# Optimization experiments

Hardware: AMD Instinct MI355X
Metric: run time of the kernel (lower is better)

The kernel has to match this reference:

```python
import jax, jax.numpy as jnp
import numpy as np

H = 16          # head_count
D = 1024        # model_dim
DPH = D // H    # dim_per_head


def setup_inputs() -> dict:
    key0 = jax.random.key(0)
    ks = jax.random.split(key0, 13)
    B, S = 4, 2048
    scale = 1.0 / np.sqrt(D)
    inp = {
        "key": jax.random.normal(ks[0], (B, S, D), jnp.float32),
        "value": jax.random.normal(ks[1], (B, S, D), jnp.float32),
        "query": jax.random.normal(ks[2], (B, S, D), jnp.float32),
        "mask": jax.random.randint(ks[3], (B, S, S), 0, 2).astype(jnp.bool_),
        "Wq": jax.random.normal(ks[4], (D, D), jnp.float32) * scale,
        "bq": jnp.zeros((D,), jnp.float32),
        "Wk": jax.random.normal(ks[5], (D, D), jnp.float32) * scale,
        "bk": jnp.zeros((D,), jnp.float32),
        "Wv": jax.random.normal(ks[6], (D, D), jnp.float32) * scale,
        "bv": jnp.zeros((D,), jnp.float32),
        "Wo": jax.random.normal(ks[7], (D, D), jnp.float32) * scale,
        "bo": jnp.zeros((D,), jnp.float32),
    }
    return inp


def _shape(x, B):
    # [B, S, D] -> [B, H, S, DPH]
    return x.reshape(B, -1, H, DPH).transpose(0, 2, 1, 3)


def reference(key, value, query, mask, Wq, bq, Wk, bk, Wv, bv, Wo, bo):
    B, S, _ = key.shape
    k_up = _shape(key @ Wk + bk, B)                       # [B,H,S,DPH]
    v_up = _shape(value @ Wv + bv, B)                     # [B,H,S,DPH]
    q_up = _shape(query @ Wq + bq, B) / jnp.sqrt(jnp.asarray(DPH, key.dtype))
    scores = jnp.einsum('bhqd,bhkd->bhqk', q_up, k_up)    # [B,H,S,S]
    scores = jnp.where(mask[:, None, :, :], jnp.asarray(-1e18, scores.dtype), scores)
    attn = jax.nn.softmax(scores, axis=-1)                # dropout = identity (eval)
    context = jnp.einsum('bhqk,bhkd->bhqd', attn, v_up)   # [B,H,S,DPH]
    context = context.transpose(0, 2, 1, 3).reshape(B, S, H * DPH)
    return context @ Wo + bo
```

## Files before the change

kernel.cpp:

```cpp
#include <hip/hip_runtime.h>

typedef _Float16 half8 __attribute__((ext_vector_type(8)));
typedef _Float16 half4 __attribute__((ext_vector_type(4)));
typedef float floatx4 __attribute__((ext_vector_type(4)));
typedef float floatx16 __attribute__((ext_vector_type(16)));

#define MFMA16(A,B,C) __builtin_amdgcn_mfma_f32_16x16x32_f16((A),(B),(C),0,0,0)
#define MFMA32(A,B,C) __builtin_amdgcn_mfma_f32_32x32x16_f16((A),(B),(C),0,0,0)


__global__ __launch_bounds__(256) void maskpack(
    const int* __restrict__ m, unsigned int* __restrict__ p)
{
  const int w = blockIdx.x * 256 + threadIdx.x;
  const int b = w >> 17;
  const int rem = w & 131071;
  const int s = rem >> 6;
  const int wp = rem & 63;
  const int4* src = (const int4*)(m + (size_t)w * 32);
  unsigned int bits = 0;
#pragma unroll
  for (int j = 0; j < 8; ++j) {
    const int4 v = src[j];
    bits |= (v.x ? 1u : 0u) << (j * 4 + 0);
    bits |= (v.y ? 1u : 0u) << (j * 4 + 1);
    bits |= (v.z ? 1u : 0u) << (j * 4 + 2);
    bits |= (v.w ? 1u : 0u) << (j * 4 + 3);
  }
  p[((size_t)(b * 64 + wp)) * 2048 + s] = bits;
}

__global__ __launch_bounds__(256) void wconv(
    const float* __restrict__ Wq, const float* __restrict__ Wk,
    const float* __restrict__ Wv, const float* __restrict__ Wo,
    _Float16* __restrict__ dst)
{
  const float* W = (blockIdx.z == 0) ? Wq : (blockIdx.z == 1) ? Wk
                  : (blockIdx.z == 2) ? Wv : Wo;
  _Float16* WT = dst + (size_t)blockIdx.z * 1024 * 1024;
  __shared__ float t[32][33];
  const int tx = threadIdx.x & 31;
  const int ty = threadIdx.x >> 5;
  const int k0 = blockIdx.x * 32, n0 = blockIdx.y * 32;
#pragma unroll
  for (int j = 0; j < 4; ++j)
    t[ty + j * 8][tx] = W[(size_t)(k0 + ty + j * 8) * 1024 + n0 + tx];
  __syncthreads();
#pragma unroll
  for (int j = 0; j < 4; ++j)
    WT[(size_t)(n0 + ty + j * 8) * 1024 + k0 + tx] = (_Float16)t[tx][ty + j * 8];
}

template <int OP>
__global__ __launch_bounds__(256) void gemm_k(
    const void* __restrict__ Ap, const _Float16* __restrict__ BT,
    const float* __restrict__ bias, void* __restrict__ Cp)
{
  __shared__ __align__(16) _Float16 As[128 * 64];
  __shared__ __align__(16) _Float16 Bs[128 * 64];
  const int tid = threadIdx.x;
  const int lane = tid & 63;
  const int wv = tid >> 6;
  const int m0 = blockIdx.x * 128;
  const int n0 = blockIdx.y * 128;
  const int wr = (wv >> 1) * 64;
  const int wc = (wv & 1) * 64;

  floatx4 acc[4][4];
#pragma unroll
  for (int i = 0; i < 4; ++i)
#pragma unroll
    for (int j = 0; j < 4; ++j) acc[i][j] = (floatx4){0.f, 0.f, 0.f, 0.f};

  char* AsB = (char*)As;
  char* BsB = (char*)Bs;

  for (int ko = 0; ko < 1024; ko += 64) {
#pragma unroll
    for (int r = 0; r < 4; ++r) {
      const int idx = (r * 256 + tid) * 8;
      const int row = idx >> 6;
      const int colh = idx & 63;
      const int dstb = row * 128 + ((colh * 2) ^ ((row & 7) << 4));
      if (OP == 3) {
        const _Float16* s = (const _Float16*)Ap + (size_t)(m0 + row) * 1024 + ko + colh;
        *(half8*)(AsB + dstb) = *(const half8*)s;
      } else {
        const float* s = (const float*)Ap + (size_t)(m0 + row) * 1024 + ko + colh;
        floatx4 v0 = *(const floatx4*)s;
        floatx4 v1 = *(const floatx4*)(s + 4);
        half8 hv;
        hv[0] = (_Float16)v0[0]; hv[1] = (_Float16)v0[1];
        hv[2] = (_Float16)v0[2]; hv[3] = (_Float16)v0[3];
        hv[4] = (_Float16)v1[0]; hv[5] = (_Float16)v1[1];
        hv[6] = (_Float16)v1[2]; hv[7] = (_Float16)v1[3];
        *(half8*)(AsB + dstb) = hv;
      }
      const _Float16* bs = BT + (size_t)(n0 + row) * 1024 + ko + colh;
      *(half8*)(BsB + dstb) = *(const half8*)bs;
    }
    __syncthreads();
#pragma unroll
    for (int kk = 0; kk < 64; kk += 32) {
      half8 af[4], bf[4];
#pragma unroll
      for (int mi = 0; mi < 4; ++mi) {
        const int row = wr + mi * 16 + (lane & 15);
        const int cb = (kk + (lane >> 4) * 8) * 2;
        af[mi] = *(const half8*)(AsB + row * 128 + (cb ^ ((row & 7) << 4)));
      }
#pragma unroll
      for (int ni = 0; ni < 4; ++ni) {
        const int row = wc + ni * 16 + (lane & 15);
        const int cb = (kk + (lane >> 4) * 8) * 2;
        bf[ni] = *(const half8*)(BsB + row * 128 + (cb ^ ((row & 7) << 4)));
      }
#pragma unroll
      for (int mi = 0; mi < 4; ++mi)
#pragma unroll
        for (int ni = 0; ni < 4; ++ni)
          acc[mi][ni] = MFMA16(af[mi], bf[ni], acc[mi][ni]);
    }
    __syncthreads();
  }

#pragma unroll
  for (int ni = 0; ni < 4; ++ni) {
    const int nn = n0 + wc + ni * 16 + (lane & 15);
    const float bvv = bias[nn];
#pragma unroll
    for (int mi = 0; mi < 4; ++mi) {
      floatx4 c = acc[mi][ni];
#pragma unroll
      for (int i = 0; i < 4; ++i) {
        const int mm = m0 + wr + mi * 16 + (lane >> 4) * 4 + i;
        float val = c[i] + bvv;
        if (OP == 0) val *= 0.1803368801111204f;
        if (OP == 0 || OP == 1) {
          _Float16* o = (_Float16*)Cp;
          const size_t off =
              ((size_t)((mm >> 11) * 16 + (nn >> 6)) * 2048 + (mm & 2047)) * 64 + (nn & 63);
          o[off] = (_Float16)val;
        } else if (OP == 2) {
          _Float16* o = (_Float16*)Cp;
          const size_t off =
              ((size_t)((mm >> 11) * 16 + (nn >> 6)) * 64 + (nn & 63)) * 2048 + (mm & 2047);
          o[off] = (_Float16)val;
        } else {
          float* o = (float*)Cp;
          o[(size_t)mm * 1024 + nn] = val;
        }
      }
    }
  }
}

__global__ __launch_bounds__(256) void attn_k(
    const _Float16* __restrict__ q_up, const _Float16* __restrict__ k_up,
    const _Float16* __restrict__ vT, const unsigned int* __restrict__ pmaskT,
    _Float16* __restrict__ ctx)
{
  const int tid = threadIdx.x;
  const int lane = tid & 63;
  const int wv = tid >> 6;
  const int bid = blockIdx.x;
  const int xcd = bid & 7;
  const int slot = bid >> 3;
  const int bh = xcd * 8 + (slot & 7);
  const int qc = slot >> 3;
  const int b = bh >> 4;
  const int h = bh & 15;
  const int l31 = lane & 31;
  const int hi = lane >> 5;
  const int qw = qc * 256 + wv * 64;

  __shared__ __align__(16) _Float16 Kl[2][32 * 64];
  __shared__ __align__(16) _Float16 Vl[2][64 * 32];

  const _Float16* qb = q_up + ((size_t)bh * 2048 + qw) * 64;
  const _Float16* kb = k_up + (size_t)bh * 2048 * 64;
  const _Float16* vb = vT + (size_t)bh * 64 * 2048;
  const unsigned int* mbase = pmaskT + (size_t)(b * 64) * 2048 + qw + l31;

  const int krow = tid >> 3, kseg = tid & 7;
  const int kByte = krow * 128 + ((kseg * 16) ^ ((krow & 7) << 4));
  const int vrow = tid >> 2, vseg = tid & 3;
  const int vByte = vrow * 64 + ((vseg * 16) ^ ((vrow & 3) << 4));
  const _Float16* gK = kb + tid * 8;
  const _Float16* gV = vb + (size_t)vrow * 2048 + vseg * 8;
  char* KB = (char*)Kl;
  char* VB = (char*)Vl;

  half8 qf[2][4];
#pragma unroll
  for (int qt = 0; qt < 2; ++qt)
#pragma unroll
    for (int kk = 0; kk < 4; ++kk)
      qf[qt][kk] = *(const half8*)(qb + (size_t)(qt * 32 + l31) * 64 + kk * 16 + hi * 8);

  floatx16 O[2][2];
#pragma unroll
  for (int qt = 0; qt < 2; ++qt)
#pragma unroll
    for (int dt = 0; dt < 2; ++dt)
#pragma unroll
      for (int r = 0; r < 16; ++r) O[qt][dt][r] = 0.f;
  float lsum[2] = {0.f, 0.f};

  half8 stK, stV;

  auto COMPUTE = [&](int buf, int t) {
    unsigned int mw[2];
    mw[0] = mbase[(size_t)t * 2048];
    mw[1] = mbase[(size_t)t * 2048 + 32];
    half8 kf[4];
#pragma unroll
    for (int kk = 0; kk < 4; ++kk)
      kf[kk] = *(const half8*)(KB + buf * 4096 + l31 * 128 +
                               ((kk * 32 + hi * 16) ^ ((l31 & 7) << 4)));
    half8 vf[2][2];
#pragma unroll
    for (int dt = 0; dt < 2; ++dt)
#pragma unroll
      for (int kk2 = 0; kk2 < 2; ++kk2)
        vf[dt][kk2] = *(const half8*)(VB + buf * 4096 + (dt * 32 + l31) * 64 +
                                      ((kk2 * 32 + hi * 16) ^ ((l31 & 3) << 4)));

    floatx16 s[2];
    __builtin_amdgcn_s_setprio(1);
#pragma unroll
    for (int qt = 0; qt < 2; ++qt) {
      floatx16 a;
#pragma unroll
      for (int r = 0; r < 16; ++r) a[r] = 0.f;
      a = MFMA32(kf[0], qf[qt][0], a);
      a = MFMA32(kf[1], qf[qt][1], a);
      a = MFMA32(kf[2], qf[qt][2], a);
      s[qt] = MFMA32(kf[3], qf[qt][3], a);
    }
    __builtin_amdgcn_s_setprio(0);

#pragma unroll
    for (int qt = 0; qt < 2; ++qt) {
      const unsigned int mh = mw[qt] >> (4 * hi);
      float e[16];
#pragma unroll
      for (int m = 0; m < 4; ++m) {
        const unsigned int bm = mh >> (8 * m);
#pragma unroll
        for (int j = 0; j < 4; ++j)
          e[4 * m + j] =
              ((bm >> j) & 1u) ? 0.f : __builtin_amdgcn_exp2f(s[qt][4 * m + j]);
      }
      float u0 = (e[0] + e[1]) + (e[2] + e[3]);
      float u1 = (e[4] + e[5]) + (e[6] + e[7]);
      float u2 = (e[8] + e[9]) + (e[10] + e[11]);
      float u3 = (e[12] + e[13]) + (e[14] + e[15]);
      lsum[qt] += (u0 + u1) + (u2 + u3);

      unsigned int c0 = __builtin_bit_cast(unsigned int, __builtin_amdgcn_cvt_pkrtz(e[0], e[1]));
      unsigned int c1 = __builtin_bit_cast(unsigned int, __builtin_amdgcn_cvt_pkrtz(e[2], e[3]));
      unsigned int c2 = __builtin_bit_cast(unsigned int, __builtin_amdgcn_cvt_pkrtz(e[4], e[5]));
      unsigned int c3 = __builtin_bit_cast(unsigned int, __builtin_amdgcn_cvt_pkrtz(e[6], e[7]));
      unsigned int c4 = __builtin_bit_cast(unsigned int, __builtin_amdgcn_cvt_pkrtz(e[8], e[9]));
      unsigned int c5 = __builtin_bit_cast(unsigned int, __builtin_amdgcn_cvt_pkrtz(e[10], e[11]));
      unsigned int c6 = __builtin_bit_cast(unsigned int, __builtin_amdgcn_cvt_pkrtz(e[12], e[13]));
      unsigned int c7 = __builtin_bit_cast(unsigned int, __builtin_amdgcn_cvt_pkrtz(e[14], e[15]));
      const unsigned int ra = __shfl_xor(hi ? c0 : c2, 32);
      const unsigned int rb = __shfl_xor(hi ? c1 : c3, 32);
      const unsigned int rc = __shfl_xor(hi ? c4 : c6, 32);
      const unsigned int rd = __shfl_xor(hi ? c5 : c7, 32);
      union { half8 v; unsigned int u[4]; } p0, p1;
      p0.u[0] = hi ? ra : c0;  p0.u[1] = hi ? rb : c1;
      p0.u[2] = hi ? c2 : ra;  p0.u[3] = hi ? c3 : rb;
      p1.u[0] = hi ? rc : c4;  p1.u[1] = hi ? rd : c5;
      p1.u[2] = hi ? c6 : rc;  p1.u[3] = hi ? c7 : rd;
      __builtin_amdgcn_s_setprio(1);
#pragma unroll
      for (int dt = 0; dt < 2; ++dt) {
        O[qt][dt] = MFMA32(vf[dt][0], p0.v, O[qt][dt]);
        O[qt][dt] = MFMA32(vf[dt][1], p1.v, O[qt][dt]);
      }
      __builtin_amdgcn_s_setprio(0);
    }
  };

  stK = *(const half8*)gK;
  stV = *(const half8*)gV;
  *(half8*)(KB + kByte) = stK;
  *(half8*)(VB + vByte) = stV;
  stK = *(const half8*)(gK + 2048);
  stV = *(const half8*)(gV + 32);
  __syncthreads();

#pragma unroll 1
  for (int t = 0; t < 64; t += 2) {
    {
      *(half8*)(KB + 4096 + kByte) = stK;
      *(half8*)(VB + 4096 + vByte) = stV;
      const int tn = (t + 2 < 64) ? t + 2 : 0;
      stK = *(const half8*)(gK + (size_t)tn * 2048);
      stV = *(const half8*)(gV + tn * 32);
      COMPUTE(0, t);
      __syncthreads();
    }
    {
      *(half8*)(KB + kByte) = stK;
      *(half8*)(VB + vByte) = stV;
      const int tn = (t + 3 < 64) ? t + 3 : 0;
      stK = *(const half8*)(gK + (size_t)tn * 2048);
      stV = *(const half8*)(gV + tn * 32);
      COMPUTE(1, t + 1);
      __syncthreads();
    }
  }

#pragma unroll
  for (int qt = 0; qt < 2; ++qt) {
    const float tot = lsum[qt] + __shfl_xor(lsum[qt], 32);
    const float inv = 1.f / tot;
    const size_t rowb = ((size_t)(b * 2048 + qw + qt * 32 + l31)) * 1024 + h * 64;
#pragma unroll
    for (int dt = 0; dt < 2; ++dt) {
#pragma unroll
      for (int m = 0; m < 4; ++m) {
        half4 w4;
        w4[0] = (_Float16)(O[qt][dt][4 * m + 0] * inv);
        w4[1] = (_Float16)(O[qt][dt][4 * m + 1] * inv);
        w4[2] = (_Float16)(O[qt][dt][4 * m + 2] * inv);
        w4[3] = (_Float16)(O[qt][dt][4 * m + 3] * inv);
        *(half4*)(ctx + rowb + dt * 32 + 8 * m + 4 * hi) = w4;
      }
    }
  }
}

extern "C" void kernel_launch(void* const* d_in, const int* in_sizes, int n_in,
                              void* d_out, int out_size, void* d_ws, size_t ws_size,
                              hipStream_t stream) {
  const float* key   = (const float*)d_in[0];
  const float* value = (const float*)d_in[1];
  const float* query = (const float*)d_in[2];
  const int*   mask  = (const int*)d_in[3];
  const float* Wq = (const float*)d_in[4];
  const float* bq = (const float*)d_in[5];
  const float* Wk = (const float*)d_in[6];
  const float* bk = (const float*)d_in[7];
  const float* Wv = (const float*)d_in[8];
  const float* bv = (const float*)d_in[9];
  const float* Wo = (const float*)d_in[10];
  const float* bo = (const float*)d_in[11];

  _Float16* wsp = (_Float16*)d_ws;
  _Float16* WT   = wsp;
  _Float16* q_up = wsp + (size_t)4 * 1024 * 1024;
  _Float16* k_up = q_up + (size_t)8192 * 1024;
  _Float16* vT   = k_up + (size_t)8192 * 1024;
  _Float16* ctx  = vT + (size_t)8192 * 1024;
  unsigned int* pmaskT = (unsigned int*)(ctx + (size_t)8192 * 1024);

  maskpack<<<dim3(2048), 256, 0, stream>>>(mask, pmaskT);
  wconv<<<dim3(32, 32, 4), 256, 0, stream>>>(Wq, Wk, Wv, Wo, WT);
  gemm_k<0><<<dim3(64, 8), 256, 0, stream>>>(query, WT, bq, q_up);
  gemm_k<1><<<dim3(64, 8), 256, 0, stream>>>(key, WT + (size_t)1024 * 1024, bk, k_up);
  gemm_k<2><<<dim3(64, 8), 256, 0, stream>>>(value, WT + (size_t)2 * 1024 * 1024, bv, vT);
  attn_k<<<dim3(512), 256, 0, stream>>>(q_up, k_up, vT, pmaskT, ctx);
  gemm_k<3><<<dim3(64, 8), 256, 0, stream>>>(ctx, WT + (size_t)3 * 1024 * 1024, bo, (float*)d_out);
}
```

Measured before the change: 289.7 us.

## Use direct global-to-LDS loads in GEMM and fix V tile swizzle

The GEMM tile loader now issues global_load_lds for the f16 B operand, and for A when it is already f16, so data goes straight into LDS instead of passing through registers. The source column is permuted per lane so the existing XOR swizzle still holds. The fp32 A path now converts with packed cvt_pkrtz instructions, which round toward zero rather than to nearest. The attention kernel's V tile swizzle is changed to a different row-bit pattern to cut LDS bank conflicts. Risks are the changed rounding of the fp32-to-f16 conversion and whether the direct-to-LDS loads are waited on correctly before the barrier.

```diff
diff --git a/kernel.cpp b/kernel.cpp
--- a/kernel.cpp
+++ b/kernel.cpp
@@ -7,6 +7,11 @@
 
 #define MFMA16(A,B,C) __builtin_amdgcn_mfma_f32_16x16x32_f16((A),(B),(C),0,0,0)
 #define MFMA32(A,B,C) __builtin_amdgcn_mfma_f32_32x32x16_f16((A),(B),(C),0,0,0)
+
+#define GLOAD_LDS(G, L)                                                        \
+  __builtin_amdgcn_global_load_lds(                                            \
+      (const __attribute__((address_space(1))) unsigned int*)(G),              \
+      (__attribute__((address_space(3))) unsigned int*)(L), 16, 0, 0)
 
 
 __global__ __launch_bounds__(256) void maskpack(
@@ -75,29 +80,39 @@
   char* AsB = (char*)As;
   char* BsB = (char*)Bs;
 
+  const int grow = lane >> 3;
+  const int gslot = (lane & 7) ^ grow;
+
   for (int ko = 0; ko < 1024; ko += 64) {
 #pragma unroll
-    for (int r = 0; r < 4; ++r) {
-      const int idx = (r * 256 + tid) * 8;
-      const int row = idx >> 6;
-      const int colh = idx & 63;
-      const int dstb = row * 128 + ((colh * 2) ^ ((row & 7) << 4));
+    for (int it = 0; it < 4; ++it) {
+      const int c = wv * 4 + it;
+      const int row = c * 8 + grow;
+      const _Float16* bsrc = BT + (size_t)(n0 + row) * 1024 + ko + gslot * 8;
+      GLOAD_LDS(bsrc, BsB + c * 1024);
       if (OP == 3) {
-        const _Float16* s = (const _Float16*)Ap + (size_t)(m0 + row) * 1024 + ko + colh;
-        *(half8*)(AsB + dstb) = *(const half8*)s;
-      } else {
+        const _Float16* asrc =
+            (const _Float16*)Ap + (size_t)(m0 + row) * 1024 + ko + gslot * 8;
+        GLOAD_LDS(asrc, AsB + c * 1024);
+      }
+    }
+    if (OP != 3) {
+#pragma unroll
+      for (int r = 0; r < 4; ++r) {
+        const int idx = (r * 256 + tid) * 8;
+        const int row = idx >> 6;
+        const int colh = idx & 63;
+        const int dstb = row * 128 + ((colh * 2) ^ ((row & 7) << 4));
         const float* s = (const float*)Ap + (size_t)(m0 + row) * 1024 + ko + colh;
         floatx4 v0 = *(const floatx4*)s;
         floatx4 v1 = *(const floatx4*)(s + 4);
-        half8 hv;
-        hv[0] = (_Float16)v0[0]; hv[1] = (_Float16)v0[1];
-        hv[2] = (_Float16)v0[2]; hv[3] = (_Float16)v0[3];
-        hv[4] = (_Float16)v1[0]; hv[5] = (_Float16)v1[1];
-        hv[6] = (_Float16)v1[2]; hv[7] = (_Float16)v1[3];
-        *(half8*)(AsB + dstb) = hv;
-      }
-      const _Float16* bs = BT + (size_t)(n0 + row) * 1024 + ko + colh;
-      *(half8*)(BsB + dstb) = *(const half8*)bs;
+        union { half8 v; unsigned int u[4]; } pk;
+        pk.u[0] = __builtin_bit_cast(unsigned int, __builtin_amdgcn_cvt_pkrtz(v0[0], v0[1]));
+        pk.u[1] = __builtin_bit_cast(unsigned int, __builtin_amdgcn_cvt_pkrtz(v0[2], v0[3]));
+        pk.u[2] = __builtin_bit_cast(unsigned int, __builtin_amdgcn_cvt_pkrtz(v1[0], v1[1]));
+        pk.u[3] = __builtin_bit_cast(unsigned int, __builtin_amdgcn_cvt_pkrtz(v1[2], v1[3]));
+        *(half8*)(AsB + dstb) = pk.v;
+      }
     }
     __syncthreads();
 #pragma unroll
@@ -185,7 +200,7 @@
   const int krow = tid >> 3, kseg = tid & 7;
   const int kByte = krow * 128 + ((kseg * 16) ^ ((krow & 7) << 4));
   const int vrow = tid >> 2, vseg = tid & 3;
-  const int vByte = vrow * 64 + ((vseg * 16) ^ ((vrow & 3) << 4));
+  const int vByte = vrow * 64 + ((vseg * 16) ^ (((vrow >> 1) & 3) << 4));
   const _Float16* gK = kb + tid * 8;
   const _Float16* gV = vb + (size_t)vrow * 2048 + vseg * 8;
   char* KB = (char*)Kl;
@@ -224,7 +239,7 @@
 #pragma unroll
       for (int kk2 = 0; kk2 < 2; ++kk2)
         vf[dt][kk2] = *(const half8*)(VB + buf * 4096 + (dt * 32 + l31) * 64 +
-                                      ((kk2 * 32 + hi * 16) ^ ((l31 & 3) << 4)));
+                                      ((kk2 * 32 + hi * 16) ^ (((l31 >> 1) & 3) << 4)));
 
     floatx16 s[2];
     __builtin_amdgcn_s_setprio(1);
```

Result: slower. 298.6 us (+3.0%).

## Permute V layout to drop cross-lane shuffles in P@V and pack conversions

Applied to the files above, without the earlier changes.

The V projection epilogue now writes the sequence index with bits 2 and 3 swapped. The P fragment from the S=K·Q MFMA output can then feed the P@V MFMA directly without __shfl_xor exchanges between lane halves, and the LDS swizzle for V is adjusted to match the new row pairing. The fp32-to-fp16 A-tile conversion in the GEMM uses packed cvt_pkrtz, and the MFMA accumulator init uses a hoisted zero vector. This removes four cross-lane shuffles and the select logic per query tile per key block, but correctness depends on the permutation matching the MFMA register layout exactly. The packed conversion also switches rounding to round-toward-zero.

```diff
diff --git a/kernel.cpp b/kernel.cpp
--- a/kernel.cpp
+++ b/kernel.cpp
@@ -89,12 +89,12 @@
         const float* s = (const float*)Ap + (size_t)(m0 + row) * 1024 + ko + colh;
         floatx4 v0 = *(const floatx4*)s;
         floatx4 v1 = *(const floatx4*)(s + 4);
-        half8 hv;
-        hv[0] = (_Float16)v0[0]; hv[1] = (_Float16)v0[1];
-        hv[2] = (_Float16)v0[2]; hv[3] = (_Float16)v0[3];
-        hv[4] = (_Float16)v1[0]; hv[5] = (_Float16)v1[1];
-        hv[6] = (_Float16)v1[2]; hv[7] = (_Float16)v1[3];
-        *(half8*)(AsB + dstb) = hv;
+        union { half8 v; unsigned int u[4]; } pk;
+        pk.u[0] = __builtin_bit_cast(unsigned int, __builtin_amdgcn_cvt_pkrtz(v0[0], v0[1]));
+        pk.u[1] = __builtin_bit_cast(unsigned int, __builtin_amdgcn_cvt_pkrtz(v0[2], v0[3]));
+        pk.u[2] = __builtin_bit_cast(unsigned int, __builtin_amdgcn_cvt_pkrtz(v1[0], v1[1]));
+        pk.u[3] = __builtin_bit_cast(unsigned int, __builtin_amdgcn_cvt_pkrtz(v1[2], v1[3]));
+        *(half8*)(AsB + dstb) = pk.v;
       }
       const _Float16* bs = BT + (size_t)(n0 + row) * 1024 + ko + colh;
       *(half8*)(BsB + dstb) = *(const half8*)bs;
@@ -143,8 +143,9 @@
           o[off] = (_Float16)val;
         } else if (OP == 2) {
           _Float16* o = (_Float16*)Cp;
+          const int mmp = (mm & ~0xC) | ((mm & 4) << 1) | ((mm & 8) >> 1);
           const size_t off =
-              ((size_t)((mm >> 11) * 16 + (nn >> 6)) * 64 + (nn & 63)) * 2048 + (mm & 2047);
+              ((size_t)((mm >> 11) * 16 + (nn >> 6)) * 64 + (nn & 63)) * 2048 + (mmp & 2047);
           o[off] = (_Float16)val;
         } else {
           float* o = (float*)Cp;
@@ -185,7 +186,7 @@
   const int krow = tid >> 3, kseg = tid & 7;
   const int kByte = krow * 128 + ((kseg * 16) ^ ((krow & 7) << 4));
   const int vrow = tid >> 2, vseg = tid & 3;
-  const int vByte = vrow * 64 + ((vseg * 16) ^ ((vrow & 3) << 4));
+  const int vByte = vrow * 64 + ((vseg * 16) ^ (((vrow >> 1) & 3) << 4));
   const _Float16* gK = kb + tid * 8;
   const _Float16* gV = vb + (size_t)vrow * 2048 + vseg * 8;
   char* KB = (char*)Kl;
@@ -206,6 +207,10 @@
 #pragma unroll
       for (int r = 0; r < 16; ++r) O[qt][dt][r] = 0.f;
   float lsum[2] = {0.f, 0.f};
+
+  floatx16 zero16;
+#pragma unroll
+  for (int r = 0; r < 16; ++r) zero16[r] = 0.f;
 
   half8 stK, stV;
 
@@ -224,16 +229,14 @@
 #pragma unroll
       for (int kk2 = 0; kk2 < 2; ++kk2)
         vf[dt][kk2] = *(const half8*)(VB + buf * 4096 + (dt * 32 + l31) * 64 +
-                                      ((kk2 * 32 + hi * 16) ^ ((l31 & 3) << 4)));
+                                      ((kk2 * 32 + hi * 16) ^ (((l31 >> 1) & 3) << 4)));
 
     floatx16 s[2];
     __builtin_amdgcn_s_setprio(1);
 #pragma unroll
     for (int qt = 0; qt < 2; ++qt) {
       floatx16 a;
-#pragma unroll
-      for (int r = 0; r < 16; ++r) a[r] = 0.f;
-      a = MFMA32(kf[0], qf[qt][0], a);
+      a = MFMA32(kf[0], qf[qt][0], zero16);
       a = MFMA32(kf[1], qf[qt][1], a);
       a = MFMA32(kf[2], qf[qt][2], a);
       s[qt] = MFMA32(kf[3], qf[qt][3], a);
@@ -258,23 +261,15 @@
       float u3 = (e[12] + e[13]) + (e[14] + e[15]);
       lsum[qt] += (u0 + u1) + (u2 + u3);
 
-      unsigned int c0 = __builtin_bit_cast(unsigned int, __builtin_amdgcn_cvt_pkrtz(e[0], e[1]));
-      unsigned int c1 = __builtin_bit_cast(unsigned int, __builtin_amdgcn_cvt_pkrtz(e[2], e[3]));
-      unsigned int c2 = __builtin_bit_cast(unsigned int, __builtin_amdgcn_cvt_pkrtz(e[4], e[5]));
-      unsigned int c3 = __builtin_bit_cast(unsigned int, __builtin_amdgcn_cvt_pkrtz(e[6], e[7]));
-      unsigned int c4 = __builtin_bit_cast(unsigned int, __builtin_amdgcn_cvt_pkrtz(e[8], e[9]));
-      unsigned int c5 = __builtin_bit_cast(unsigned int, __builtin_amdgcn_cvt_pkrtz(e[10], e[11]));
-      unsigned int c6 = __builtin_bit_cast(unsigned int, __builtin_amdgcn_cvt_pkrtz(e[12], e[13]));
-      unsigned int c7 = __builtin_bit_cast(unsigned int, __builtin_amdgcn_cvt_pkrtz(e[14], e[15]));
-      const unsigned int ra = __shfl_xor(hi ? c0 : c2, 32);
-      const unsigned int rb = __shfl_xor(hi ? c1 : c3, 32);
-      const unsigned int rc = __shfl_xor(hi ? c4 : c6, 32);
-      const unsigned int rd = __shfl_xor(hi ? c5 : c7, 32);
       union { half8 v; unsigned int u[4]; } p0, p1;
-      p0.u[0] = hi ? ra : c0;  p0.u[1] = hi ? rb : c1;
-      p0.u[2] = hi ? c2 : ra;  p0.u[3] = hi ? c3 : rb;
-      p1.u[0] = hi ? rc : c4;  p1.u[1] = hi ? rd : c5;
-      p1.u[2] = hi ? c6 : rc;  p1.u[3] = hi ? c7 : rd;
+      p0.u[0] = __builtin_bit_cast(unsigned int, __builtin_amdgcn_cvt_pkrtz(e[0], e[1]));
+      p0.u[1] = __builtin_bit_cast(unsigned int, __builtin_amdgcn_cvt_pkrtz(e[2], e[3]));
+      p0.u[2] = __builtin_bit_cast(unsigned int, __builtin_amdgcn_cvt_pkrtz(e[4], e[5]));
+      p0.u[3] = __builtin_bit_cast(unsigned int, __builtin_amdgcn_cvt_pkrtz(e[6], e[7]));
+      p1.u[0] = __builtin_bit_cast(unsigned int, __builtin_amdgcn_cvt_pkrtz(e[8], e[9]));
+      p1.u[1] = __builtin_bit_cast(unsigned int, __builtin_amdgcn_cvt_pkrtz(e[10], e[11]));
+      p1.u[2] = __builtin_bit_cast(unsigned int, __builtin_amdgcn_cvt_pkrtz(e[12], e[13]));
+      p1.u[3] = __builtin_bit_cast(unsigned int, __builtin_amdgcn_cvt_pkrtz(e[14], e[15]));
       __builtin_amdgcn_s_setprio(1);
 #pragma unroll
       for (int dt = 0; dt < 2; ++dt) {
```

Result: faster. 276.2 us (-4.7%).
